# Kernel tuning notes

Hardware: AMD Instinct MI355X
Metric: run time of the kernel (lower is better)

Reference implementation:

```python
import jax, jax.numpy as jnp
import numpy as np

N_NODES = 100000
N_EDGES = 3200000
IN_CH, HID_CH, OUT_CH = 128, 64, 40


def gcn_conv(x, row, col, norm, W, b, n_nodes):
    # linear transform first (PyG GCNConv order), then normalized aggregation
    h = x @ W                                   # [N, out]
    msg = h[row] * norm[:, None]                # [E+N, out] gathered & scaled
    out = jax.ops.segment_sum(msg, col, num_segments=n_nodes)
    return out + b


def setup_inputs() -> dict:
    key = jax.random.key(0)
    k0, k1, k2, k3, k4, k5 = jax.random.split(key, 6)
    x = jax.random.normal(k0, (N_NODES, IN_CH), dtype=jnp.float32)
    edge_index = jax.random.randint(k1, (2, N_EDGES), 0, N_NODES, dtype=jnp.int64)
    # Glorot-ish init for weights
    W1 = jax.random.normal(k2, (IN_CH, HID_CH), dtype=jnp.float32) * (1.0 / np.sqrt(IN_CH))
    b1 = jnp.zeros((HID_CH,), dtype=jnp.float32)
    W2 = jax.random.normal(k3, (HID_CH, OUT_CH), dtype=jnp.float32) * (1.0 / np.sqrt(HID_CH))
    b2 = jnp.zeros((OUT_CH,), dtype=jnp.float32)
    return {"x": x, "edge_index": edge_index, "original_size": N_NODES,
            "W1": W1, "b1": b1, "W2": W2, "b2": b2}


def reference(x, edge_index, original_size, W1, b1, W2, b2):
    n = x.shape[0]
    # add self-loops (GCNConv default)
    loops = jnp.arange(n, dtype=edge_index.dtype)
    row = jnp.concatenate([edge_index[0], loops])   # source
    col = jnp.concatenate([edge_index[1], loops])   # target
    # symmetric normalization: deg over targets with unit edge weights
    deg = jax.ops.segment_sum(jnp.ones_like(col, dtype=x.dtype), col, num_segments=n)
    dinv = jnp.where(deg > 0, jax.lax.rsqrt(deg), 0.0)
    norm = dinv[row] * dinv[col]                    # [E+N]
    h = gcn_conv(x, row, col, norm, W1, b1, n)
    h = gcn_conv(h, row, col, norm, W2, b2, n)
    out = jax.nn.log_softmax(h, axis=1)
    return out[:original_size]
```

## Files before the change

kernel.cpp:

```cpp
#include <hip/hip_runtime.h>
#include <math.h>


#define NN 100000
#define NE 3200000
#define NBUK 391
#define BCAP 8704
#define EPB 16384


__global__ void k_zero(int* __restrict__ p, int n) {
  int i = blockIdx.x * blockDim.x + threadIdx.x;
  if (i < n) p[i] = 0;
}


__device__ __forceinline__ unsigned bf16rne(float x) {
  unsigned u = __float_as_uint(x);
  return (u + 0x7fffu + ((u >> 16) & 1u)) >> 16;
}
__device__ __forceinline__ unsigned pack2(float lo, float hi) {
  return bf16rne(lo) | (bf16rne(hi) << 16);
}


__global__ __launch_bounds__(256) void k_bucket(const int* __restrict__ ei,
                                                int* __restrict__ tail,
                                                unsigned* __restrict__ bucket) {
  __shared__ int hist[NBUK], wbase[NBUK], loc[NBUK];
  const int tid = threadIdx.x;
  const int beg = blockIdx.x * EPB;
  const int end = min(beg + EPB, NE);
  const int* col = ei + NE;
  for (int b = tid; b < NBUK; b += 256) { hist[b] = 0; loc[b] = 0; }
  __syncthreads();
  for (int e = beg + tid * 4; e < end; e += 1024) {
    int4 c4 = *(const int4*)(col + e);
    atomicAdd(&hist[c4.x >> 8], 1);
    atomicAdd(&hist[c4.y >> 8], 1);
    atomicAdd(&hist[c4.z >> 8], 1);
    atomicAdd(&hist[c4.w >> 8], 1);
  }
  __syncthreads();
  for (int b = tid; b < NBUK; b += 256)
    wbase[b] = atomicAdd(&tail[b], hist[b]);
  __syncthreads();
  for (int e = beg + tid * 4; e < end; e += 1024) {
    int4 c4 = *(const int4*)(col + e);
    int4 r4 = *(const int4*)(ei + e);
    {
      int b = c4.x >> 8;
      unsigned pos = (unsigned)(wbase[b] + atomicAdd(&loc[b], 1));
      if (pos < BCAP) bucket[(size_t)b * BCAP + pos] = ((unsigned)r4.x << 8) | (unsigned)(c4.x & 255);
    }
    {
      int b = c4.y >> 8;
      unsigned pos = (unsigned)(wbase[b] + atomicAdd(&loc[b], 1));
      if (pos < BCAP) bucket[(size_t)b * BCAP + pos] = ((unsigned)r4.y << 8) | (unsigned)(c4.y & 255);
    }
    {
      int b = c4.z >> 8;
      unsigned pos = (unsigned)(wbase[b] + atomicAdd(&loc[b], 1));
      if (pos < BCAP) bucket[(size_t)b * BCAP + pos] = ((unsigned)r4.z << 8) | (unsigned)(c4.z & 255);
    }
    {
      int b = c4.w >> 8;
      unsigned pos = (unsigned)(wbase[b] + atomicAdd(&loc[b], 1));
      if (pos < BCAP) bucket[(size_t)b * BCAP + pos] = ((unsigned)r4.w << 8) | (unsigned)(c4.w & 255);
    }
  }
}


__global__ void k_bstart(const int* __restrict__ tail, int* __restrict__ bstart) {
  const int tid = threadIdx.x, lane = tid & 63, wid = tid >> 6;
  int v = (tid < NBUK) ? min(tail[tid], BCAP) : 0;
  int s = v;
  #pragma unroll
  for (int d = 1; d < 64; d <<= 1) { int t = __shfl_up(s, d, 64); if (lane >= d) s += t; }
  __shared__ int wsum[8];
  if (lane == 63) wsum[wid] = s;
  __syncthreads();
  int wpre = 0;
  for (int w = 0; w < wid; ++w) wpre += wsum[w];
  int excl = wpre + s - v;
  if (tid <= NBUK) bstart[tid] = excl;
}


__global__ __launch_bounds__(256) void k_sort(const unsigned* __restrict__ bucket,
                                              const int* __restrict__ tail,
                                              const int* __restrict__ bstart,
                                              int* __restrict__ csr_src,
                                              int* __restrict__ offsets,
                                              float* __restrict__ dinv) {
  __shared__ int h[256], base_[256], loc[256];
  __shared__ int sorted[BCAP];
  __shared__ int wsum[4];
  const int b = blockIdx.x;
  const int lo = b << 8;
  const int nc = min(256, NN - lo);
  const int n = min(tail[b], BCAP);
  const int seg0 = bstart[b];
  const unsigned* __restrict__ bk = bucket + (size_t)b * BCAP;
  const int tid = threadIdx.x, lane = tid & 63, wid = tid >> 6;
  h[tid] = 0; loc[tid] = 0;
  __syncthreads();
  int i = tid * 4;
  for (; i + 3 < n; i += 1024) {
    uint4 v = *(const uint4*)(bk + i);
    atomicAdd(&h[v.x & 255u], 1);
    atomicAdd(&h[v.y & 255u], 1);
    atomicAdd(&h[v.z & 255u], 1);
    atomicAdd(&h[v.w & 255u], 1);
  }
  for (; i < n; ++i) atomicAdd(&h[bk[i] & 255u], 1);
  __syncthreads();
  {
    int v = h[tid];
    int s = v;
    #pragma unroll
    for (int d = 1; d < 64; d <<= 1) { int t = __shfl_up(s, d, 64); if (lane >= d) s += t; }
    if (lane == 63) wsum[wid] = s;
    __syncthreads();
    int wpre = 0;
    #pragma unroll
    for (int w = 0; w < 4; ++w) if (w < wid) wpre += wsum[w];
    int excl = wpre + s - v;
    base_[tid] = excl;
    if (tid < nc) {
      dinv[lo + tid] = rsqrtf((float)(v + 1));
      offsets[lo + tid] = seg0 + excl;
    }
  }
  if (b == 0 && tid == 0) offsets[NN] = bstart[NBUK];
  __syncthreads();
  i = tid * 4;
  for (; i + 3 < n; i += 1024) {
    uint4 v = *(const uint4*)(bk + i);
    { int c = v.x & 255u; sorted[base_[c] + atomicAdd(&loc[c], 1)] = (int)(v.x >> 8); }
    { int c = v.y & 255u; sorted[base_[c] + atomicAdd(&loc[c], 1)] = (int)(v.y >> 8); }
    { int c = v.z & 255u; sorted[base_[c] + atomicAdd(&loc[c], 1)] = (int)(v.z >> 8); }
    { int c = v.w & 255u; sorted[base_[c] + atomicAdd(&loc[c], 1)] = (int)(v.w >> 8); }
  }
  for (; i < n; ++i) {
    unsigned ent = bk[i];
    int c = ent & 255u;
    sorted[base_[c] + atomicAdd(&loc[c], 1)] = (int)(ent >> 8);
  }
  __syncthreads();
  for (int t = tid; t < n; t += 256) csr_src[seg0 + t] = sorted[t];
}


__global__ __launch_bounds__(256) void k_gemm1(const float* __restrict__ x,
                                               const float* __restrict__ W1,
                                               const float* __restrict__ dinv,
                                               unsigned* __restrict__ m1b) {
  __shared__ float ws[128 * 64];
  __shared__ float xs[16 * 132];
  const int tid = threadIdx.x;
  for (int k = tid; k < 128 * 64; k += 256) ws[k] = W1[k];
  const int row0 = blockIdx.x * 16;
  for (int k = tid; k < 16 * 128; k += 256)
    xs[(k >> 7) * 132 + (k & 127)] = x[row0 * 128 + k];
  __syncthreads();
  const int cg = tid & 15;
  const int r = tid >> 4;
  const float4* __restrict__ xr4 = (const float4*)(xs + r * 132);
  const float4* __restrict__ ws4 = (const float4*)ws;
  float4 acc = make_float4(0.f, 0.f, 0.f, 0.f);
  #pragma unroll 8
  for (int k4 = 0; k4 < 32; ++k4) {
    float4 xv = xr4[k4];
    float4 w0 = ws4[(k4 * 4 + 0) * 16 + cg];
    float4 w1 = ws4[(k4 * 4 + 1) * 16 + cg];
    float4 w2 = ws4[(k4 * 4 + 2) * 16 + cg];
    float4 w3 = ws4[(k4 * 4 + 3) * 16 + cg];
    acc.x = fmaf(xv.x, w0.x, fmaf(xv.y, w1.x, fmaf(xv.z, w2.x, fmaf(xv.w, w3.x, acc.x))));
    acc.y = fmaf(xv.x, w0.y, fmaf(xv.y, w1.y, fmaf(xv.z, w2.y, fmaf(xv.w, w3.y, acc.y))));
    acc.z = fmaf(xv.x, w0.z, fmaf(xv.y, w1.z, fmaf(xv.z, w2.z, fmaf(xv.w, w3.z, acc.z))));
    acc.w = fmaf(xv.x, w0.w, fmaf(xv.y, w1.w, fmaf(xv.z, w2.w, fmaf(xv.w, w3.w, acc.w))));
  }
  const float d = dinv[row0 + r];
  uint2 o;
  o.x = pack2(acc.x * d, acc.y * d);
  o.y = pack2(acc.z * d, acc.w * d);
  ((uint2*)m1b)[(row0 + r) * 16 + cg] = o;
}


#define ACC8(v, f)                                                   \
  acc[0] = fmaf(__uint_as_float((v).x << 16), (f), acc[0]);          \
  acc[1] = fmaf(__uint_as_float((v).x & 0xffff0000u), (f), acc[1]);  \
  acc[2] = fmaf(__uint_as_float((v).y << 16), (f), acc[2]);          \
  acc[3] = fmaf(__uint_as_float((v).y & 0xffff0000u), (f), acc[3]);  \
  acc[4] = fmaf(__uint_as_float((v).z << 16), (f), acc[4]);          \
  acc[5] = fmaf(__uint_as_float((v).z & 0xffff0000u), (f), acc[5]);  \
  acc[6] = fmaf(__uint_as_float((v).w << 16), (f), acc[6]);          \
  acc[7] = fmaf(__uint_as_float((v).w & 0xffff0000u), (f), acc[7]);


__global__ __launch_bounds__(256) void k_agg1(const unsigned* __restrict__ m1b,
                                              const int* __restrict__ offsets,
                                              const int* __restrict__ csr_src,
                                              const float* __restrict__ dinv,
                                              const float* __restrict__ b1,
                                              float* __restrict__ a1) {
  const int node = blockIdx.x * 4 + (threadIdx.x >> 6);
  const int lane = threadIdx.x & 63;
  const int e = lane >> 3;
  const int q = lane & 7;
  const uint4* __restrict__ m1v = (const uint4*)m1b;
  const int beg = offsets[node], end = offsets[node + 1];
  float acc[8];
  #pragma unroll
  for (int j = 0; j < 8; ++j) acc[j] = 0.f;
  for (int p = beg; p < end; p += 32) {
    const int i0 = p + e, i1 = p + 8 + e, i2 = p + 16 + e, i3 = p + 24 + e;
    const int s0 = csr_src[i0 < end ? i0 : beg];
    const int s1 = csr_src[i1 < end ? i1 : beg];
    const int s2 = csr_src[i2 < end ? i2 : beg];
    const int s3 = csr_src[i3 < end ? i3 : beg];
    const float f0 = (i0 < end) ? 1.f : 0.f;
    const float f1 = (i1 < end) ? 1.f : 0.f;
    const float f2 = (i2 < end) ? 1.f : 0.f;
    const float f3 = (i3 < end) ? 1.f : 0.f;
    uint4 v0 = m1v[s0 * 8 + q];
    uint4 v1 = m1v[s1 * 8 + q];
    uint4 v2 = m1v[s2 * 8 + q];
    uint4 v3 = m1v[s3 * 8 + q];
    ACC8(v0, f0);
    ACC8(v1, f1);
    ACC8(v2, f2);
    ACC8(v3, f3);
  }
  #pragma unroll
  for (int j = 0; j < 8; ++j) {
    acc[j] += __shfl_xor(acc[j], 8, 64);
    acc[j] += __shfl_xor(acc[j], 16, 64);
    acc[j] += __shfl_xor(acc[j], 32, 64);
  }
  if (e == 0) {
    uint4 sv = m1v[node * 8 + q];
    const float d = dinv[node];
    float4 bb0 = ((const float4*)b1)[q * 2];
    float4 bb1 = ((const float4*)b1)[q * 2 + 1];
    float4 o0, o1;
    o0.x = (acc[0] + __uint_as_float(sv.x << 16)) * d + bb0.x;
    o0.y = (acc[1] + __uint_as_float(sv.x & 0xffff0000u)) * d + bb0.y;
    o0.z = (acc[2] + __uint_as_float(sv.y << 16)) * d + bb0.z;
    o0.w = (acc[3] + __uint_as_float(sv.y & 0xffff0000u)) * d + bb0.w;
    o1.x = (acc[4] + __uint_as_float(sv.z << 16)) * d + bb1.x;
    o1.y = (acc[5] + __uint_as_float(sv.z & 0xffff0000u)) * d + bb1.y;
    o1.z = (acc[6] + __uint_as_float(sv.w << 16)) * d + bb1.z;
    o1.w = (acc[7] + __uint_as_float(sv.w & 0xffff0000u)) * d + bb1.w;
    ((float4*)a1)[node * 16 + q * 2] = o0;
    ((float4*)a1)[node * 16 + q * 2 + 1] = o1;
  }
}


__global__ __launch_bounds__(256) void k_gemm2(const float* __restrict__ a1,
                                               const float* __restrict__ W2,
                                               const float* __restrict__ dinv,
                                               unsigned* __restrict__ m2b) {
  __shared__ float ws[64 * 40];
  const int tid = threadIdx.x;
  for (int k = tid; k < 64 * 40; k += 256) ws[k] = W2[k];
  __syncthreads();
  const int idx = blockIdx.x * 256 + tid;
  if (idx >= NN * 20) return;
  const int node = idx / 20;
  const int c0 = (idx - node * 20) * 2;
  const float4* __restrict__ a4 = (const float4*)(a1 + node * 64);
  float acc0 = 0.f, acc1 = 0.f;
  #pragma unroll
  for (int k4 = 0; k4 < 16; ++k4) {
    float4 a = a4[k4];
    acc0 = fmaf(a.x, ws[(k4 * 4 + 0) * 40 + c0], acc0);
    acc1 = fmaf(a.x, ws[(k4 * 4 + 0) * 40 + c0 + 1], acc1);
    acc0 = fmaf(a.y, ws[(k4 * 4 + 1) * 40 + c0], acc0);
    acc1 = fmaf(a.y, ws[(k4 * 4 + 1) * 40 + c0 + 1], acc1);
    acc0 = fmaf(a.z, ws[(k4 * 4 + 2) * 40 + c0], acc0);
    acc1 = fmaf(a.z, ws[(k4 * 4 + 2) * 40 + c0 + 1], acc1);
    acc0 = fmaf(a.w, ws[(k4 * 4 + 3) * 40 + c0], acc0);
    acc1 = fmaf(a.w, ws[(k4 * 4 + 3) * 40 + c0 + 1], acc1);
  }
  const float d = dinv[node];
  m2b[idx] = pack2(acc0 * d, acc1 * d);
}


__device__ __forceinline__ float shfl1(float v, int src) {
  return __shfl(v, src & 63, 64);
}

__global__ __launch_bounds__(256) void k_agg2(const unsigned* __restrict__ m2b,
                                              const int* __restrict__ offsets,
                                              const int* __restrict__ csr_src,
                                              const float* __restrict__ dinv,
                                              const float* __restrict__ b2,
                                              float* __restrict__ out) {
  const int node = blockIdx.x * 4 + (threadIdx.x >> 6);
  const int lane = threadIdx.x & 63;
  const bool act = lane < 60;
  const int e = act ? (lane / 5) : 0;
  const int q = act ? (lane - e * 5) : 0;
  const uint4* __restrict__ m2v = (const uint4*)m2b;
  const int beg = offsets[node], end = offsets[node + 1];
  float acc[8];
  #pragma unroll
  for (int j = 0; j < 8; ++j) acc[j] = 0.f;
  for (int p = beg; p < end; p += 48) {
    const int i0 = p + e, i1 = p + 12 + e, i2 = p + 24 + e, i3 = p + 36 + e;
    const int s0 = csr_src[i0 < end ? i0 : beg];
    const int s1 = csr_src[i1 < end ? i1 : beg];
    const int s2 = csr_src[i2 < end ? i2 : beg];
    const int s3 = csr_src[i3 < end ? i3 : beg];
    const float f0 = (act && i0 < end) ? 1.f : 0.f;
    const float f1 = (act && i1 < end) ? 1.f : 0.f;
    const float f2 = (act && i2 < end) ? 1.f : 0.f;
    const float f3 = (act && i3 < end) ? 1.f : 0.f;
    uint4 v0 = m2v[s0 * 5 + q];
    uint4 v1 = m2v[s1 * 5 + q];
    uint4 v2 = m2v[s2 * 5 + q];
    uint4 v3 = m2v[s3 * 5 + q];
    ACC8(v0, f0);
    ACC8(v1, f1);
    ACC8(v2, f2);
    ACC8(v3, f3);
  }
  #pragma unroll
  for (int j = 0; j < 8; ++j) acc[j] += shfl1(acc[j], lane + 30);
  #pragma unroll
  for (int j = 0; j < 8; ++j) acc[j] += shfl1(acc[j], lane + 15);
  #pragma unroll
  for (int j = 0; j < 8; ++j) {
    float t1 = shfl1(acc[j], lane + 5);
    float t2 = shfl1(acc[j], lane + 10);
    acc[j] += t1 + t2;
  }
  const bool lead = (lane < 5);
  float r[8];
  #pragma unroll
  for (int j = 0; j < 8; ++j) r[j] = 0.f;
  if (lead) {
    uint4 sv = m2v[node * 5 + lane];
    const float d = dinv[node];
    float4 bb0 = ((const float4*)b2)[lane * 2];
    float4 bb1 = ((const float4*)b2)[lane * 2 + 1];
    r[0] = (acc[0] + __uint_as_float(sv.x << 16)) * d + bb0.x;
    r[1] = (acc[1] + __uint_as_float(sv.x & 0xffff0000u)) * d + bb0.y;
    r[2] = (acc[2] + __uint_as_float(sv.y << 16)) * d + bb0.z;
    r[3] = (acc[3] + __uint_as_float(sv.y & 0xffff0000u)) * d + bb0.w;
    r[4] = (acc[4] + __uint_as_float(sv.z << 16)) * d + bb1.x;
    r[5] = (acc[5] + __uint_as_float(sv.z & 0xffff0000u)) * d + bb1.y;
    r[6] = (acc[6] + __uint_as_float(sv.w << 16)) * d + bb1.z;
    r[7] = (acc[7] + __uint_as_float(sv.w & 0xffff0000u)) * d + bb1.w;
  }
  float mx = -INFINITY;
  if (lead) {
    mx = fmaxf(fmaxf(fmaxf(r[0], r[1]), fmaxf(r[2], r[3])),
               fmaxf(fmaxf(r[4], r[5]), fmaxf(r[6], r[7])));
  }
  #pragma unroll
  for (int d = 4; d > 0; d >>= 1) mx = fmaxf(mx, __shfl_xor(mx, d, 8));
  float se = 0.f;
  if (lead) {
    se = __expf(r[0] - mx) + __expf(r[1] - mx) + __expf(r[2] - mx) +
         __expf(r[3] - mx) + __expf(r[4] - mx) + __expf(r[5] - mx) +
         __expf(r[6] - mx) + __expf(r[7] - mx);
  }
  #pragma unroll
  for (int d = 4; d > 0; d >>= 1) se += __shfl_xor(se, d, 8);
  if (lead) {
    const float lse = mx + logf(se);
    float4 o0, o1;
    o0.x = r[0] - lse; o0.y = r[1] - lse; o0.z = r[2] - lse; o0.w = r[3] - lse;
    o1.x = r[4] - lse; o1.y = r[5] - lse; o1.z = r[6] - lse; o1.w = r[7] - lse;
    ((float4*)out)[node * 10 + lane * 2] = o0;
    ((float4*)out)[node * 10 + lane * 2 + 1] = o1;
  }
}


extern "C" void kernel_launch(void* const* d_in, const int* in_sizes, int n_in,
                              void* d_out, int out_size, void* d_ws, size_t ws_size,
                              hipStream_t stream) {
  const float* x   = (const float*)d_in[0];
  const int*   ei  = (const int*)d_in[1];
  const float* W1  = (const float*)d_in[3];
  const float* b1  = (const float*)d_in[4];
  const float* W2  = (const float*)d_in[5];
  const float* b2  = (const float*)d_in[6];
  float*       out = (float*)d_out;

  char* ws = (char*)d_ws;
  int*      tail    = (int*)(ws + 0);
  int*      bstart  = (int*)(ws + (size_t)4 * 1024);
  int*      offsets = (int*)(ws + (size_t)8 * 1024);
  float*    dinv    = (float*)(ws + (size_t)512 * 1024);
  int*      csr_src = (int*)(ws + (size_t)1024 * 1024);
  unsigned* bucket  = (unsigned*)(ws + (size_t)14 * 1024 * 1024);
  unsigned* m1b     = (unsigned*)(ws + (size_t)14 * 1024 * 1024);
  float*    a1      = (float*)(ws + (size_t)40 * 1024 * 1024);
  unsigned* m2b     = m1b;

  k_zero<<<2, 256, 0, stream>>>(tail, NBUK);
  k_bucket<<<(NE + EPB - 1) / EPB, 256, 0, stream>>>(ei, tail, bucket);
  k_bstart<<<1, 512, 0, stream>>>(tail, bstart);
  k_sort<<<NBUK, 256, 0, stream>>>(bucket, tail, bstart, csr_src, offsets, dinv);
  k_gemm1<<<NN / 16, 256, 0, stream>>>(x, W1, dinv, m1b);
  k_agg1<<<NN / 4, 256, 0, stream>>>(m1b, offsets, csr_src, dinv, b1, a1);
  k_gemm2<<<(NN * 20 + 255) / 256, 256, 0, stream>>>(a1, W2, dinv, m2b);
  k_agg2<<<NN / 4, 256, 0, stream>>>(m2b, offsets, csr_src, dinv, b2, out);
}
```

Baseline: 237.4 us.

## Register-block first GEMM with 8x8 per-thread tiles over 128-row blocks

Rewrites the x@W1 kernel so that each 128-thread block handles 128 rows. Each thread computes an 8x8 output tile held in registers, while x is staged transposed into shared memory in K-slices of 16. The old version reloaded all of W1 into LDS for every 16 rows; the new one amortizes that load over 128 rows and raises FMA-to-LDS-load ratio. The trade-offs are higher register pressure, fewer blocks, and extra syncs per K-slice.

```diff
diff --git a/kernel.cpp b/kernel.cpp
--- a/kernel.cpp
+++ b/kernel.cpp
@@ -153,40 +153,72 @@
 }
 
 
-__global__ __launch_bounds__(256) void k_gemm1(const float* __restrict__ x,
+__global__ __launch_bounds__(128) void k_gemm1(const float* __restrict__ x,
                                                const float* __restrict__ W1,
                                                const float* __restrict__ dinv,
                                                unsigned* __restrict__ m1b) {
   __shared__ float ws[128 * 64];
-  __shared__ float xs[16 * 132];
+  __shared__ float xt[16 * 132];
   const int tid = threadIdx.x;
-  for (int k = tid; k < 128 * 64; k += 256) ws[k] = W1[k];
-  const int row0 = blockIdx.x * 16;
-  for (int k = tid; k < 16 * 128; k += 256)
-    xs[(k >> 7) * 132 + (k & 127)] = x[row0 * 128 + k];
-  __syncthreads();
-  const int cg = tid & 15;
-  const int r = tid >> 4;
-  const float4* __restrict__ xr4 = (const float4*)(xs + r * 132);
+  const int row0 = blockIdx.x * 128;
+  {
+    const float4* __restrict__ w4 = (const float4*)W1;
+    float4* __restrict__ s4 = (float4*)ws;
+    for (int i = tid; i < 128 * 16; i += 128) s4[i] = w4[i];
+  }
+  const int cg = tid & 7;
+  const int rg = tid >> 3;
+  const int lr = tid >> 2;
+  const int lk = tid & 3;
+  float acc[8][8];
+  #pragma unroll
+  for (int i = 0; i < 8; ++i)
+    #pragma unroll
+    for (int j = 0; j < 8; ++j) acc[i][j] = 0.f;
+  const float4* __restrict__ xt4 = (const float4*)xt;
   const float4* __restrict__ ws4 = (const float4*)ws;
-  float4 acc = make_float4(0.f, 0.f, 0.f, 0.f);
-  #pragma unroll 8
-  for (int k4 = 0; k4 < 32; ++k4) {
-    float4 xv = xr4[k4];
-    float4 w0 = ws4[(k4 * 4 + 0) * 16 + cg];
-    float4 w1 = ws4[(k4 * 4 + 1) * 16 + cg];
-    float4 w2 = ws4[(k4 * 4 + 2) * 16 + cg];
-    float4 w3 = ws4[(k4 * 4 + 3) * 16 + cg];
-    acc.x = fmaf(xv.x, w0.x, fmaf(xv.y, w1.x, fmaf(xv.z, w2.x, fmaf(xv.w, w3.x, acc.x))));
-    acc.y = fmaf(xv.x, w0.y, fmaf(xv.y, w1.y, fmaf(xv.z, w2.y, fmaf(xv.w, w3.y, acc.y))));
-    acc.z = fmaf(xv.x, w0.z, fmaf(xv.y, w1.z, fmaf(xv.z, w2.z, fmaf(xv.w, w3.z, acc.z))));
-    acc.w = fmaf(xv.x, w0.w, fmaf(xv.y, w1.w, fmaf(xv.z, w2.w, fmaf(xv.w, w3.w, acc.w))));
-  }
-  const float d = dinv[row0 + r];
-  uint2 o;
-  o.x = pack2(acc.x * d, acc.y * d);
-  o.y = pack2(acc.z * d, acc.w * d);
-  ((uint2*)m1b)[(row0 + r) * 16 + cg] = o;
+  for (int ks = 0; ks < 8; ++ks) {
+    __syncthreads();
+    #pragma unroll
+    for (int it = 0; it < 4; ++it) {
+      const int row = it * 32 + lr;
+      int grow = row0 + row; if (grow > NN - 1) grow = NN - 1;
+      float4 v = *(const float4*)(x + (size_t)grow * 128 + ks * 16 + lk * 4);
+      xt[(lk * 4 + 0) * 132 + row] = v.x;
+      xt[(lk * 4 + 1) * 132 + row] = v.y;
+      xt[(lk * 4 + 2) * 132 + row] = v.z;
+      xt[(lk * 4 + 3) * 132 + row] = v.w;
+    }
+    __syncthreads();
+    #pragma unroll 2
+    for (int kk = 0; kk < 16; ++kk) {
+      const int k = ks * 16 + kk;
+      float4 xa = xt4[kk * 33 + rg * 2];
+      float4 xb = xt4[kk * 33 + rg * 2 + 1];
+      float4 wa = ws4[k * 16 + cg * 2];
+      float4 wb = ws4[k * 16 + cg * 2 + 1];
+      float xr[8] = {xa.x, xa.y, xa.z, xa.w, xb.x, xb.y, xb.z, xb.w};
+      float wc[8] = {wa.x, wa.y, wa.z, wa.w, wb.x, wb.y, wb.z, wb.w};
+      #pragma unroll
+      for (int i = 0; i < 8; ++i)
+        #pragma unroll
+        for (int j = 0; j < 8; ++j)
+          acc[i][j] = fmaf(xr[i], wc[j], acc[i][j]);
+    }
+  }
+  #pragma unroll
+  for (int i = 0; i < 8; ++i) {
+    const int row = row0 + rg * 8 + i;
+    if (row < NN) {
+      const float d = dinv[row];
+      uint4 o;
+      o.x = pack2(acc[i][0] * d, acc[i][1] * d);
+      o.y = pack2(acc[i][2] * d, acc[i][3] * d);
+      o.z = pack2(acc[i][4] * d, acc[i][5] * d);
+      o.w = pack2(acc[i][6] * d, acc[i][7] * d);
+      ((uint4*)m1b)[row * 8 + cg] = o;
+    }
+  }
 }
 
 
@@ -411,7 +443,7 @@
   k_bucket<<<(NE + EPB - 1) / EPB, 256, 0, stream>>>(ei, tail, bucket);
   k_bstart<<<1, 512, 0, stream>>>(tail, bstart);
   k_sort<<<NBUK, 256, 0, stream>>>(bucket, tail, bstart, csr_src, offsets, dinv);
-  k_gemm1<<<NN / 16, 256, 0, stream>>>(x, W1, dinv, m1b);
+  k_gemm1<<<(NN + 127) / 128, 128, 0, stream>>>(x, W1, dinv, m1b);
   k_agg1<<<NN / 4, 256, 0, stream>>>(m1b, offsets, csr_src, dinv, b1, a1);
   k_gemm2<<<(NN * 20 + 255) / 256, 256, 0, stream>>>(a1, W2, dinv, m2b);
   k_agg2<<<NN / 4, 256, 0, stream>>>(m2b, offsets, csr_src, dinv, b2, out);
```

New measurement: 233.1 us. About the same (-1.8%).
